# Kernel tuning notes

Measured on AMD Instinct MI355X. Metric: run time of the kernel, lower is better.

Reference implementation:

```python
import jax, jax.numpy as jnp
import numpy as np

TOTAL_WORDS = 10000
EMBED_LEN = 100
SEQ_LEN = 80
UNITS = 512
BATCH = 1024


def gru_layer(x_seq, Wx, Wh, b):
    """Keras GRU (reset_after=True), x_seq: [T, B, D] -> ys: [T, B, U]."""
    bi, br = b[0], b[1]  # input bias, recurrent bias, each [3U]
    U = Wh.shape[0]

    def step(h, x_t):
        gx = x_t @ Wx + bi            # [B, 3U]
        gh = h @ Wh + br              # [B, 3U]
        xz, xr, xh = gx[:, :U], gx[:, U:2 * U], gx[:, 2 * U:]
        hz, hr, hn = gh[:, :U], gh[:, U:2 * U], gh[:, 2 * U:]
        z = jax.nn.sigmoid(xz + hz)
        r = jax.nn.sigmoid(xr + hr)
        hh = jnp.tanh(xh + r * hn)
        h_new = z * h + (1.0 - z) * hh
        return h_new, h_new

    h0 = jnp.zeros((x_seq.shape[1], U), dtype=x_seq.dtype)
    _, ys = jax.lax.scan(step, h0, x_seq)
    return ys


def setup_inputs() -> dict:
    key = jax.random.key(0)
    ks = jax.random.split(key, 10)
    tokens = jax.random.randint(ks[0], (BATCH, SEQ_LEN), 0, TOTAL_WORDS, dtype=jnp.int32)
    s_e = 1.0 / np.sqrt(EMBED_LEN)
    s_u = 1.0 / np.sqrt(UNITS)
    emb = jax.random.normal(ks[1], (TOTAL_WORDS, EMBED_LEN), jnp.float32) * 0.05
    Wx1 = jax.random.normal(ks[2], (EMBED_LEN, 3 * UNITS), jnp.float32) * s_e
    Wh1 = jax.random.normal(ks[3], (UNITS, 3 * UNITS), jnp.float32) * s_u
    b1 = jnp.zeros((2, 3 * UNITS), jnp.float32)
    Wx2 = jax.random.normal(ks[4], (UNITS, 3 * UNITS), jnp.float32) * s_u
    Wh2 = jax.random.normal(ks[5], (UNITS, 3 * UNITS), jnp.float32) * s_u
    b2 = jnp.zeros((2, 3 * UNITS), jnp.float32)
    Wfc = jax.random.normal(ks[6], (UNITS, 1), jnp.float32) * s_u
    bfc = jnp.zeros((1,), jnp.float32)
    return {"tokens": tokens, "emb": emb, "Wx1": Wx1, "Wh1": Wh1, "b1": b1,
            "Wx2": Wx2, "Wh2": Wh2, "b2": b2, "Wfc": Wfc, "bfc": bfc}


def reference(tokens, emb, Wx1, Wh1, b1, Wx2, Wh2, b2, Wfc, bfc):
    x = emb[tokens]                       # [B, T, E]
    x = jnp.transpose(x, (1, 0, 2))       # [T, B, E] (scan over time)
    ys1 = gru_layer(x, Wx1, Wh1, b1)      # [T, B, U] return_sequences
    ys2 = gru_layer(ys1, Wx2, Wh2, b2)    # [T, B, U]
    h_last = ys2[-1]                      # [B, U] (last timestep only)
    logits = h_last @ Wfc + bfc           # [B, 1]
    return jax.nn.sigmoid(logits)
```

## Files before the change

kernel.cpp:

```cpp
#include <hip/hip_runtime.h>
#include <hip/hip_bf16.h>
#include <math.h>

typedef float f32x4 __attribute__((ext_vector_type(4)));
typedef int   ix4  __attribute__((ext_vector_type(4)));

#define MFMAI8(a,b,c) __builtin_amdgcn_mfma_i32_16x16x64_i8(a,b,c,0,0,0)

constexpr int BATCH = 1024, SEQ = 80, EMB = 100, U = 512;
constexpr int KC1 = 10;
constexpr int KC2 = 16;
constexpr float EMBMAX = 0.32f;
constexpr float INV127SQ = 1.f / 16129.f;

__device__ __forceinline__ float sigf_(float x) {
  return __builtin_amdgcn_rcpf(1.f + __expf(-x));
}
__device__ __forceinline__ float tanhf_(float x) {
  return fmaf(2.f, __builtin_amdgcn_rcpf(1.f + __expf(-2.f * x)), -1.f);
}

__global__ void k_colmax(const float* __restrict__ Wh1, const float* __restrict__ Wx1,
                         const float* __restrict__ Wh2, const float* __restrict__ Wx2,
                         float* __restrict__ scales) {
  int idx = blockIdx.x * 256 + threadIdx.x;
  if (idx >= 4 * 8 * 1536) return;
  int col = idx % 1536;
  int rest = idx / 1536;
  int kseg = rest & 7, m = rest >> 3;
  const float* W = (m == 0) ? Wh1 : (m == 1) ? Wx1 : (m == 2) ? Wh2 : Wx2;
  int Klim = (m == 1) ? EMB : 512;
  int k0 = kseg * 64, k1 = min(k0 + 64, Klim);
  float mx = 0.f;
  for (int k = k0; k < k1; ++k) mx = fmaxf(mx, fabsf(W[(size_t)k * 1536 + col]));
  if (k1 > k0) atomicMax((int*)&scales[m * 1536 + col], __float_as_int(mx));
}

__global__ void k_pack_i8(const float* __restrict__ WH, const float* __restrict__ WX,
                          const float* __restrict__ scH, const float* __restrict__ scX,
                          signed char* __restrict__ out, int KCH, int KCX, int KXr) {
  int c = blockIdx.x * 256 + threadIdx.x;
  int KC = KCH + KCX;
  if (c >= 32 * KC * 3 * 64) return;
  int lane = c & 63;
  int rest = c >> 6;
  int g = rest % 3; rest /= 3;
  int kc = rest % KC;
  int lb = rest / KC;
  int col = g * 512 + lb * 16 + (lane & 15);
  int kl = (lane >> 4) * 16;
  float sH = 127.f / fmaxf(scH[col], 1e-12f);
  float sX = 127.f / fmaxf(scX[col], 1e-12f);
  ix4 v;
  signed char* vb = (signed char*)&v;
#pragma unroll
  for (int e = 0; e < 16; ++e) {
    int q = 0;
    if (kc < KCH) {
      int k = kc * 64 + kl + e;
      q = (int)rintf(WH[(size_t)k * 1536 + col] * sH);
    } else {
      int kx = (kc - KCH) * 64 + kl + e;
      if (kx < KXr) q = (int)rintf(WX[(size_t)kx * 1536 + col] * sX);
    }
    vb[e] = (signed char)q;
  }
  *(ix4*)(out + (size_t)c * 16) = v;
}

__global__ void k_emb_quant(const float* __restrict__ in, signed char* __restrict__ out) {
  int idx = blockIdx.x * 256 + threadIdx.x;
  if (idx >= 10000 * 128) return;
  int r = idx >> 7, c = idx & 127;
  int q = 0;
  if (c < EMB) {
    float x = in[r * EMB + c] * (127.f / EMBMAX);
    q = (int)rintf(fminf(127.f, fmaxf(-127.f, x)));
  }
  out[idx] = (signed char)q;
}

__device__ __forceinline__ unsigned llc_read(unsigned* p) {
  unsigned v;
  asm volatile("global_load_dword %0, %1, off sc0 sc1\n\ts_waitcnt vmcnt(0)"
               : "=v"(v) : "v"(p) : "memory");
  return v;
}

__device__ __forceinline__ void bar_slow(unsigned* cnt, unsigned tgt) {
  __syncthreads();
  if (threadIdx.x == 0) {
    __builtin_amdgcn_fence(__ATOMIC_RELEASE, "agent");
    __hip_atomic_fetch_add(cnt, 1u, __ATOMIC_RELAXED, __HIP_MEMORY_SCOPE_AGENT);
    while (__hip_atomic_fetch_add(cnt, 0u, __ATOMIC_RELAXED, __HIP_MEMORY_SCOPE_AGENT) < tgt)
      __builtin_amdgcn_s_sleep(1);
    __builtin_amdgcn_fence(__ATOMIC_ACQUIRE, "agent");
  }
  __syncthreads();
}

__device__ __forceinline__ void bar_fast(unsigned* cnt, unsigned tgt) {
  asm volatile("s_waitcnt vmcnt(0)" ::: "memory");
  __syncthreads();
  if (threadIdx.x == 0) {
    __hip_atomic_fetch_add(cnt, 1u, __ATOMIC_RELAXED, __HIP_MEMORY_SCOPE_AGENT);
    while (llc_read(cnt) < tgt) __builtin_amdgcn_s_sleep(1);
    asm volatile("buffer_inv sc0\n\ts_waitcnt vmcnt(0)" ::: "memory");
  }
  __syncthreads();
}

__global__ __launch_bounds__(512, 2)
void k_gru_persist(const int* __restrict__ tokens, const signed char* __restrict__ embq,
                   const signed char* __restrict__ wf1, const signed char* __restrict__ wf2,
                   const float* __restrict__ b1, const float* __restrict__ b2,
                   const float* __restrict__ scales,
                   signed char* __restrict__ h1b0, signed char* __restrict__ h1b1,
                   signed char* __restrict__ h2b0, signed char* __restrict__ h2b1,
                   const float* __restrict__ Wfc, const float* __restrict__ bfc,
                   float* __restrict__ out, unsigned* __restrict__ bar) {
  __shared__ __attribute__((aligned(16))) signed char wt1[KC1 * 3 * 1024];
  __shared__ __attribute__((aligned(16))) signed char wt2[KC2 * 3 * 1024];
  __shared__ int fastsh;

  const int bid = blockIdx.x, tid = threadIdx.x;
  const int g = bid & 7, lb = bid >> 3;
  const int u0 = lb * 16, r0 = g * 128;
  unsigned* cnt = bar + g * 64;
  unsigned* xslot = bar + 512;

  {
    const ix4* s1 = (const ix4*)(wf1 + (size_t)lb * KC1 * 3 * 1024);
    ix4* d1 = (ix4*)wt1;
    for (int i = tid; i < KC1 * 3 * 64; i += 512) d1[i] = s1[i];
    const ix4* s2 = (const ix4*)(wf2 + (size_t)lb * KC2 * 3 * 1024);
    ix4* d2 = (ix4*)wt2;
    for (int i = tid; i < KC2 * 3 * 64; i += 512) d2[i] = s2[i];
  }

  {
    unsigned xcc = 0;
    asm volatile("s_getreg_b32 %0, hwreg(HW_REG_XCC_ID)" : "=s"(xcc));
    if (tid == 0)
      __hip_atomic_store(&xslot[bid], xcc + 1u, __ATOMIC_RELAXED, __HIP_MEMORY_SCOPE_AGENT);
    bar_slow(cnt, 32u);
    if (tid == 0) {
      unsigned x0 = __hip_atomic_load(&xslot[g], __ATOMIC_RELAXED, __HIP_MEMORY_SCOPE_AGENT);
      int f = (x0 != 0u);
      for (int i = 1; i < 32; ++i)
        f &= (__hip_atomic_load(&xslot[i * 8 + g], __ATOMIC_RELAXED, __HIP_MEMORY_SCOPE_AGENT) == x0);
      fastsh = f;
    }
    __syncthreads();
  }
  const bool fastbar = (fastsh != 0);

  const int wv = tid >> 6, lane = tid & 63, ln = lane & 15, quad = lane >> 4;
  const int rw0 = r0 + wv * 16;
  const int lofs = lane * 16;
  const int kq = quad * 16;

  const int u = u0 + ln;
  const float* sc_h1 = scales, *sc_x1 = scales + 1536, *sc_h2 = scales + 3072, *sc_x2 = scales + 4608;
  const float fz1h = sc_h1[u] * INV127SQ,        fz1x = sc_x1[u] * (EMBMAX * INV127SQ);
  const float fr1h = sc_h1[512 + u] * INV127SQ,  fr1x = sc_x1[512 + u] * (EMBMAX * INV127SQ);
  const float fn1h = sc_h1[1024 + u] * INV127SQ, fn1x = sc_x1[1024 + u] * (EMBMAX * INV127SQ);
  const float fz2h = sc_h2[u] * INV127SQ,        fz2x = sc_x2[u] * INV127SQ;
  const float fr2h = sc_h2[512 + u] * INV127SQ,  fr2x = sc_x2[512 + u] * INV127SQ;
  const float fn2h = sc_h2[1024 + u] * INV127SQ, fn2x = sc_x2[1024 + u] * INV127SQ;
  const float bz1 = b1[u] + b1[1536 + u],       br1 = b1[512 + u] + b1[2048 + u];
  const float bn1x = b1[1024 + u],              bn1h = b1[2560 + u];
  const float bz2 = b2[u] + b2[1536 + u],       br2 = b2[512 + u] + b2[2048 + u];
  const float bn2x = b2[1024 + u],              bn2h = b2[2560 + u];
  const size_t wb8 = (size_t)(u >> 6) * 65536 + (u & 63);

  float h1st[4] = {0.f, 0.f, 0.f, 0.f};
  float h2st[4] = {0.f, 0.f, 0.f, 0.f};
  unsigned tgt = 64u;

#pragma unroll 1
  for (int s = 0; s <= SEQ; ++s) {
    const signed char* h1r = (s & 1) ? h1b0 : h1b1;
    signed char*       h1w = (s & 1) ? h1b1 : h1b0;
    const signed char* h2r = (s & 1) ? h2b1 : h2b0;
    signed char*       h2w = (s & 1) ? h2b0 : h2b1;

    ix4 z1h, z1x, r1h, r1x, n1h, n1x, z2h, z2x, r2h, r2x, n2h, n2x;
    z1h = z1x = r1h = r1x = n1h = n1x = (ix4){0, 0, 0, 0};
    z2h = z2x = r2h = r2x = n2h = n2x = (ix4){0, 0, 0, 0};

#pragma unroll
    for (int kc = 0; kc < 8; ++kc) {
      ix4 a = *(const ix4*)(h1r + (size_t)kc * 65536 + (rw0 + ln) * 64 + kq);
      z1h = MFMAI8(a, *(const ix4*)(wt1 + (kc * 3 + 0) * 1024 + lofs), z1h);
      r1h = MFMAI8(a, *(const ix4*)(wt1 + (kc * 3 + 1) * 1024 + lofs), r1h);
      n1h = MFMAI8(a, *(const ix4*)(wt1 + (kc * 3 + 2) * 1024 + lofs), n1h);
      z2x = MFMAI8(a, *(const ix4*)(wt2 + ((8 + kc) * 3 + 0) * 1024 + lofs), z2x);
      r2x = MFMAI8(a, *(const ix4*)(wt2 + ((8 + kc) * 3 + 1) * 1024 + lofs), r2x);
      n2x = MFMAI8(a, *(const ix4*)(wt2 + ((8 + kc) * 3 + 2) * 1024 + lofs), n2x);
    }
#pragma unroll
    for (int kc = 0; kc < 8; ++kc) {
      ix4 a = *(const ix4*)(h2r + (size_t)kc * 65536 + (rw0 + ln) * 64 + kq);
      z2h = MFMAI8(a, *(const ix4*)(wt2 + (kc * 3 + 0) * 1024 + lofs), z2h);
      r2h = MFMAI8(a, *(const ix4*)(wt2 + (kc * 3 + 1) * 1024 + lofs), r2h);
      n2h = MFMAI8(a, *(const ix4*)(wt2 + (kc * 3 + 2) * 1024 + lofs), n2h);
    }
    {
      int se = (s < SEQ) ? s : SEQ - 1;
      int tok = tokens[(size_t)(rw0 + ln) * SEQ + se];
#pragma unroll
      for (int kc = 0; kc < 2; ++kc) {
        ix4 a = *(const ix4*)(embq + (size_t)tok * 128 + kc * 64 + kq);
        z1x = MFMAI8(a, *(const ix4*)(wt1 + ((8 + kc) * 3 + 0) * 1024 + lofs), z1x);
        r1x = MFMAI8(a, *(const ix4*)(wt1 + ((8 + kc) * 3 + 1) * 1024 + lofs), r1x);
        n1x = MFMAI8(a, *(const ix4*)(wt1 + ((8 + kc) * 3 + 2) * 1024 + lofs), n1x);
      }
    }

    if (s < SEQ) {
#pragma unroll
      for (int i = 0; i < 4; ++i) {
        int row = rw0 + quad * 4 + i;
        float z = sigf_(fmaf(fz1h, (float)z1h[i], fmaf(fz1x, (float)z1x[i], bz1)));
        float r = sigf_(fmaf(fr1h, (float)r1h[i], fmaf(fr1x, (float)r1x[i], br1)));
        float hh = tanhf_(fmaf(fn1x, (float)n1x[i], bn1x) +
                          r * fmaf(fn1h, (float)n1h[i], bn1h));
        float hn = hh + z * (h1st[i] - hh);
        h1st[i] = hn;
        h1w[wb8 + (size_t)row * 64] = (signed char)(int)rintf(hn * 127.f);
      }
    }
    if (s >= 1) {
#pragma unroll
      for (int i = 0; i < 4; ++i) {
        int row = rw0 + quad * 4 + i;
        float z = sigf_(fmaf(fz2h, (float)z2h[i], fmaf(fz2x, (float)z2x[i], bz2)));
        float r = sigf_(fmaf(fr2h, (float)r2h[i], fmaf(fr2x, (float)r2x[i], br2)));
        float hh = tanhf_(fmaf(fn2x, (float)n2x[i], bn2x) +
                          r * fmaf(fn2h, (float)n2h[i], bn2h));
        float hn = hh + z * (h2st[i] - hh);
        h2st[i] = hn;
        h2w[wb8 + (size_t)row * 64] = (signed char)(int)rintf(hn * 127.f);
      }
    }

    if (fastbar) bar_fast(cnt, tgt);
    else         bar_slow(cnt, tgt);
    tgt += 32u;
  }

  if (lb < 8) {
    int row = r0 + lb * 16 + wv * 2 + (lane >> 5);
    int l32 = lane & 31;
    float sfc = 0.f;
#pragma unroll
    for (int k = l32; k < U; k += 32)
      sfc += (float)h2b1[(size_t)(k >> 6) * 65536 + row * 64 + (k & 63)] * Wfc[k];
#pragma unroll
    for (int off = 16; off; off >>= 1) sfc += __shfl_down(sfc, off, 32);
    if (l32 == 0) out[row] = sigf_(sfc * (1.f / 127.f) + bfc[0]);
  }
}

extern "C" void kernel_launch(void* const* d_in, const int* in_sizes, int n_in,
                              void* d_out, int out_size, void* d_ws, size_t ws_size,
                              hipStream_t stream) {
  const int*   tokens = (const int*)d_in[0];
  const float* emb = (const float*)d_in[1];
  const float* Wx1 = (const float*)d_in[2];
  const float* Wh1 = (const float*)d_in[3];
  const float* b1  = (const float*)d_in[4];
  const float* Wx2 = (const float*)d_in[5];
  const float* Wh2 = (const float*)d_in[6];
  const float* b2  = (const float*)d_in[7];
  const float* Wfc = (const float*)d_in[8];
  const float* bfc = (const float*)d_in[9];
  float* out = (float*)d_out;

  signed char* wf1  = (signed char*)d_ws;
  signed char* wf2  = wf1 + 983040;
  signed char* embq = wf2 + 1572864;
  float* scales     = (float*)(embq + 1280000);
  signed char* h1b0 = (signed char*)scales + 24576;
  signed char* h1b1 = h1b0 + 524288;
  signed char* h2b0 = h1b1 + 524288;
  signed char* h2b1 = h2b0 + 524288;
  unsigned* bar = (unsigned*)(h2b1 + 524288);

  hipMemsetAsync(scales, 0, 24576 + (size_t)4 * 524288 + 3072, stream);

  k_colmax<<<(4 * 8 * 1536 + 255) / 256, 256, 0, stream>>>(Wh1, Wx1, Wh2, Wx2, scales);
  k_pack_i8<<<(32 * KC1 * 3 * 64 + 255) / 256, 256, 0, stream>>>(
      Wh1, Wx1, scales, scales + 1536, wf1, 8, 2, EMB);
  k_pack_i8<<<(32 * KC2 * 3 * 64 + 255) / 256, 256, 0, stream>>>(
      Wh2, Wx2, scales + 3072, scales + 4608, wf2, 8, 8, U);
  k_emb_quant<<<(10000 * 128 + 255) / 256, 256, 0, stream>>>(emb, embq);

  void* args[] = {(void*)&tokens, (void*)&embq, (void*)&wf1, (void*)&wf2,
                  (void*)&b1, (void*)&b2, (void*)&scales,
                  (void*)&h1b0, (void*)&h1b1, (void*)&h2b0, (void*)&h2b1,
                  (void*)&Wfc, (void*)&bfc, (void*)&out, (void*)&bar};
  hipLaunchCooperativeKernel((void*)k_gru_persist, dim3(256), dim3(512), args, 0, stream);
}
```

Baseline: 579.0 us.

## Repartition persistent GRU into 16 row-groups, keep layer-1 weights in registers, fuse prep kernels

The persistent kernel now uses 16 batch-row groups of 64 rows, each with 16 blocks, in place of 8 groups of 128 rows with 32 blocks. Each wave covers one of two 16-unit slices, so a block caches two layer-2 weight slices in LDS. Layer-1 weights (30 fragments) move into VGPRs instead of LDS, and each barrier group shrinks to 16 blocks. The three prep kernels (two packs and the embedding quantize) merge into one launch, the embedding quantize writes 4 bytes per thread, and the kernel zeroes the h1 initial buffer itself so the large memset shrinks. The aim is fewer participants per grid barrier, less LDS traffic for layer 1 and fewer launches, at the cost of register pressure that could reduce occupancy under launch_bounds(512,2).

```diff
diff --git a/kernel.cpp b/kernel.cpp
--- a/kernel.cpp
+++ b/kernel.cpp
@@ -36,18 +36,19 @@
   if (k1 > k0) atomicMax((int*)&scales[m * 1536 + col], __float_as_int(mx));
 }
 
-__global__ void k_pack_i8(const float* __restrict__ WH, const float* __restrict__ WX,
-                          const float* __restrict__ scH, const float* __restrict__ scX,
-                          signed char* __restrict__ out, int KCH, int KCX, int KXr) {
-  int c = blockIdx.x * 256 + threadIdx.x;
+__device__ __forceinline__ void pack_one(const float* __restrict__ WH,
+                                         const float* __restrict__ WX,
+                                         const float* __restrict__ scH,
+                                         const float* __restrict__ scX,
+                                         signed char* __restrict__ out,
+                                         int KCH, int KCX, int KXr, int c) {
   int KC = KCH + KCX;
-  if (c >= 32 * KC * 3 * 64) return;
   int lane = c & 63;
   int rest = c >> 6;
   int g = rest % 3; rest /= 3;
   int kc = rest % KC;
-  int lb = rest / KC;
-  int col = g * 512 + lb * 16 + (lane & 15);
+  int u16 = rest / KC;
+  int col = g * 512 + u16 * 16 + (lane & 15);
   int kl = (lane >> 4) * 16;
   float sH = 127.f / fmaxf(scH[col], 1e-12f);
   float sX = 127.f / fmaxf(scX[col], 1e-12f);
@@ -68,16 +69,35 @@
   *(ix4*)(out + (size_t)c * 16) = v;
 }
 
-__global__ void k_emb_quant(const float* __restrict__ in, signed char* __restrict__ out) {
-  int idx = blockIdx.x * 256 + threadIdx.x;
-  if (idx >= 10000 * 128) return;
-  int r = idx >> 7, c = idx & 127;
-  int q = 0;
-  if (c < EMB) {
-    float x = in[r * EMB + c] * (127.f / EMBMAX);
-    q = (int)rintf(fminf(127.f, fmaxf(-127.f, x)));
-  }
-  out[idx] = (signed char)q;
+__global__ void k_prep(const float* __restrict__ Wh1, const float* __restrict__ Wx1,
+                       const float* __restrict__ Wh2, const float* __restrict__ Wx2,
+                       const float* __restrict__ scales,
+                       signed char* __restrict__ wf1, signed char* __restrict__ wf2,
+                       const float* __restrict__ emb, signed char* __restrict__ embq) {
+  int b = blockIdx.x, tid = threadIdx.x;
+  if (b < 240) {
+    int c = b * 256 + tid;
+    if (c < 61440) pack_one(Wh1, Wx1, scales, scales + 1536, wf1, 8, 2, EMB, c);
+  } else if (b < 624) {
+    int c = (b - 240) * 256 + tid;
+    if (c < 98304) pack_one(Wh2, Wx2, scales + 3072, scales + 4608, wf2, 8, 8, U, c);
+  } else {
+    int idx = (b - 624) * 256 + tid;
+    if (idx < 320000) {
+      int r = idx >> 5, c4 = (idx & 31) * 4;
+      char q[4];
+#pragma unroll
+      for (int j = 0; j < 4; ++j) {
+        int c = c4 + j, v = 0;
+        if (c < EMB) {
+          float x = emb[r * EMB + c] * (127.f / EMBMAX);
+          v = (int)rintf(fminf(127.f, fmaxf(-127.f, x)));
+        }
+        q[j] = (char)v;
+      }
+      *(int*)(embq + (size_t)r * 128 + c4) = *(int*)q;
+    }
+  }
 }
 
 __device__ __forceinline__ unsigned llc_read(unsigned* p) {
@@ -119,48 +139,58 @@
                    signed char* __restrict__ h2b0, signed char* __restrict__ h2b1,
                    const float* __restrict__ Wfc, const float* __restrict__ bfc,
                    float* __restrict__ out, unsigned* __restrict__ bar) {
-  __shared__ __attribute__((aligned(16))) signed char wt1[KC1 * 3 * 1024];
-  __shared__ __attribute__((aligned(16))) signed char wt2[KC2 * 3 * 1024];
+  __shared__ __attribute__((aligned(16))) signed char wt2[2 * KC2 * 3 * 1024];
   __shared__ int fastsh;
 
   const int bid = blockIdx.x, tid = threadIdx.x;
-  const int g = bid & 7, lb = bid >> 3;
-  const int u0 = lb * 16, r0 = g * 128;
+  const int g = bid & 15, lb = bid >> 4;
+  const int r0 = g * 64;
   unsigned* cnt = bar + g * 64;
-  unsigned* xslot = bar + 512;
+  unsigned* xslot = bar + 1024;
 
   {
-    const ix4* s1 = (const ix4*)(wf1 + (size_t)lb * KC1 * 3 * 1024);
-    ix4* d1 = (ix4*)wt1;
-    for (int i = tid; i < KC1 * 3 * 64; i += 512) d1[i] = s1[i];
-    const ix4* s2 = (const ix4*)(wf2 + (size_t)lb * KC2 * 3 * 1024);
+    ix4* hz = (ix4*)(h1b0 + (size_t)bid * 8192);
+    hz[tid] = (ix4){0, 0, 0, 0};
+  }
+
+  {
+    const ix4* s2 = (const ix4*)(wf2 + (size_t)lb * 6144 * 16);
     ix4* d2 = (ix4*)wt2;
-    for (int i = tid; i < KC2 * 3 * 64; i += 512) d2[i] = s2[i];
-  }
+    for (int i = tid; i < 6144; i += 512) d2[i] = s2[i];
+  }
+
+  const int wv = tid >> 6, lane = tid & 63, ln = lane & 15, quad = lane >> 4;
+  const int rt = wv >> 1, uh = wv & 1;
+  const int u16 = lb * 2 + uh;
+  const int rw0 = r0 + rt * 16;
+  const int kq = quad * 16;
+
+  ix4 w1[30];
+  {
+    const ix4* s1 = (const ix4*)(wf1 + (size_t)u16 * KC1 * 3 * 1024);
+#pragma unroll
+    for (int f = 0; f < 30; ++f) w1[f] = s1[f * 64 + lane];
+  }
+  const signed char* wt2h = wt2 + uh * (KC2 * 3 * 1024) + lane * 16;
 
   {
     unsigned xcc = 0;
     asm volatile("s_getreg_b32 %0, hwreg(HW_REG_XCC_ID)" : "=s"(xcc));
     if (tid == 0)
       __hip_atomic_store(&xslot[bid], xcc + 1u, __ATOMIC_RELAXED, __HIP_MEMORY_SCOPE_AGENT);
-    bar_slow(cnt, 32u);
+    bar_slow(cnt, 16u);
     if (tid == 0) {
       unsigned x0 = __hip_atomic_load(&xslot[g], __ATOMIC_RELAXED, __HIP_MEMORY_SCOPE_AGENT);
       int f = (x0 != 0u);
-      for (int i = 1; i < 32; ++i)
-        f &= (__hip_atomic_load(&xslot[i * 8 + g], __ATOMIC_RELAXED, __HIP_MEMORY_SCOPE_AGENT) == x0);
+      for (int j = 1; j < 16; ++j)
+        f &= (__hip_atomic_load(&xslot[g + 16 * j], __ATOMIC_RELAXED, __HIP_MEMORY_SCOPE_AGENT) == x0);
       fastsh = f;
     }
     __syncthreads();
   }
   const bool fastbar = (fastsh != 0);
 
-  const int wv = tid >> 6, lane = tid & 63, ln = lane & 15, quad = lane >> 4;
-  const int rw0 = r0 + wv * 16;
-  const int lofs = lane * 16;
-  const int kq = quad * 16;
-
-  const int u = u0 + ln;
+  const int u = u16 * 16 + ln;
   const float* sc_h1 = scales, *sc_x1 = scales + 1536, *sc_h2 = scales + 3072, *sc_x2 = scales + 4608;
   const float fz1h = sc_h1[u] * INV127SQ,        fz1x = sc_x1[u] * (EMBMAX * INV127SQ);
   const float fr1h = sc_h1[512 + u] * INV127SQ,  fr1x = sc_x1[512 + u] * (EMBMAX * INV127SQ);
@@ -176,7 +206,7 @@
 
   float h1st[4] = {0.f, 0.f, 0.f, 0.f};
   float h2st[4] = {0.f, 0.f, 0.f, 0.f};
-  unsigned tgt = 64u;
+  unsigned tgt = 32u;
 
 #pragma unroll 1
   for (int s = 0; s <= SEQ; ++s) {
@@ -192,19 +222,19 @@
 #pragma unroll
     for (int kc = 0; kc < 8; ++kc) {
       ix4 a = *(const ix4*)(h1r + (size_t)kc * 65536 + (rw0 + ln) * 64 + kq);
-      z1h = MFMAI8(a, *(const ix4*)(wt1 + (kc * 3 + 0) * 1024 + lofs), z1h);
-      r1h = MFMAI8(a, *(const ix4*)(wt1 + (kc * 3 + 1) * 1024 + lofs), r1h);
-      n1h = MFMAI8(a, *(const ix4*)(wt1 + (kc * 3 + 2) * 1024 + lofs), n1h);
-      z2x = MFMAI8(a, *(const ix4*)(wt2 + ((8 + kc) * 3 + 0) * 1024 + lofs), z2x);
-      r2x = MFMAI8(a, *(const ix4*)(wt2 + ((8 + kc) * 3 + 1) * 1024 + lofs), r2x);
-      n2x = MFMAI8(a, *(const ix4*)(wt2 + ((8 + kc) * 3 + 2) * 1024 + lofs), n2x);
+      z1h = MFMAI8(a, w1[kc * 3 + 0], z1h);
+      r1h = MFMAI8(a, w1[kc * 3 + 1], r1h);
+      n1h = MFMAI8(a, w1[kc * 3 + 2], n1h);
+      z2x = MFMAI8(a, *(const ix4*)(wt2h + ((8 + kc) * 3 + 0) * 1024), z2x);
+      r2x = MFMAI8(a, *(const ix4*)(wt2h + ((8 + kc) * 3 + 1) * 1024), r2x);
+      n2x = MFMAI8(a, *(const ix4*)(wt2h + ((8 + kc) * 3 + 2) * 1024), n2x);
     }
 #pragma unroll
     for (int kc = 0; kc < 8; ++kc) {
       ix4 a = *(const ix4*)(h2r + (size_t)kc * 65536 + (rw0 + ln) * 64 + kq);
-      z2h = MFMAI8(a, *(const ix4*)(wt2 + (kc * 3 + 0) * 1024 + lofs), z2h);
-      r2h = MFMAI8(a, *(const ix4*)(wt2 + (kc * 3 + 1) * 1024 + lofs), r2h);
-      n2h = MFMAI8(a, *(const ix4*)(wt2 + (kc * 3 + 2) * 1024 + lofs), n2h);
+      z2h = MFMAI8(a, *(const ix4*)(wt2h + (kc * 3 + 0) * 1024), z2h);
+      r2h = MFMAI8(a, *(const ix4*)(wt2h + (kc * 3 + 1) * 1024), r2h);
+      n2h = MFMAI8(a, *(const ix4*)(wt2h + (kc * 3 + 2) * 1024), n2h);
     }
     {
       int se = (s < SEQ) ? s : SEQ - 1;
@@ -212,9 +242,9 @@
 #pragma unroll
       for (int kc = 0; kc < 2; ++kc) {
         ix4 a = *(const ix4*)(embq + (size_t)tok * 128 + kc * 64 + kq);
-        z1x = MFMAI8(a, *(const ix4*)(wt1 + ((8 + kc) * 3 + 0) * 1024 + lofs), z1x);
-        r1x = MFMAI8(a, *(const ix4*)(wt1 + ((8 + kc) * 3 + 1) * 1024 + lofs), r1x);
-        n1x = MFMAI8(a, *(const ix4*)(wt1 + ((8 + kc) * 3 + 2) * 1024 + lofs), n1x);
+        z1x = MFMAI8(a, w1[(8 + kc) * 3 + 0], z1x);
+        r1x = MFMAI8(a, w1[(8 + kc) * 3 + 1], r1x);
+        n1x = MFMAI8(a, w1[(8 + kc) * 3 + 2], n1x);
       }
     }
 
@@ -247,19 +277,20 @@
 
     if (fastbar) bar_fast(cnt, tgt);
     else         bar_slow(cnt, tgt);
-    tgt += 32u;
-  }
-
-  if (lb < 8) {
-    int row = r0 + lb * 16 + wv * 2 + (lane >> 5);
-    int l32 = lane & 31;
+    tgt += 16u;
+  }
+
+  if (wv < 4) {
+    int row = r0 + lb * 4 + wv;
     float sfc = 0.f;
 #pragma unroll
-    for (int k = l32; k < U; k += 32)
-      sfc += (float)h2b1[(size_t)(k >> 6) * 65536 + row * 64 + (k & 63)] * Wfc[k];
-#pragma unroll
-    for (int off = 16; off; off >>= 1) sfc += __shfl_down(sfc, off, 32);
-    if (l32 == 0) out[row] = sigf_(sfc * (1.f / 127.f) + bfc[0]);
+    for (int j = 0; j < 8; ++j) {
+      int k = j * 64 + lane;
+      sfc += (float)h2b1[(size_t)j * 65536 + row * 64 + lane] * Wfc[k];
+    }
+#pragma unroll
+    for (int off = 32; off; off >>= 1) sfc += __shfl_down(sfc, off, 64);
+    if (lane == 0) out[row] = sigf_(sfc * (1.f / 127.f) + bfc[0]);
   }
 }
 
@@ -282,20 +313,16 @@
   signed char* wf2  = wf1 + 983040;
   signed char* embq = wf2 + 1572864;
   float* scales     = (float*)(embq + 1280000);
-  signed char* h1b0 = (signed char*)scales + 24576;
+  unsigned* bar     = (unsigned*)((signed char*)scales + 24576);
+  signed char* h1b0 = (signed char*)bar + 8192;
   signed char* h1b1 = h1b0 + 524288;
   signed char* h2b0 = h1b1 + 524288;
   signed char* h2b1 = h2b0 + 524288;
-  unsigned* bar = (unsigned*)(h2b1 + 524288);
-
-  hipMemsetAsync(scales, 0, 24576 + (size_t)4 * 524288 + 3072, stream);
+
+  hipMemsetAsync(scales, 0, 24576 + 8192, stream);
 
   k_colmax<<<(4 * 8 * 1536 + 255) / 256, 256, 0, stream>>>(Wh1, Wx1, Wh2, Wx2, scales);
-  k_pack_i8<<<(32 * KC1 * 3 * 64 + 255) / 256, 256, 0, stream>>>(
-      Wh1, Wx1, scales, scales + 1536, wf1, 8, 2, EMB);
-  k_pack_i8<<<(32 * KC2 * 3 * 64 + 255) / 256, 256, 0, stream>>>(
-      Wh2, Wx2, scales + 3072, scales + 4608, wf2, 8, 8, U);
-  k_emb_quant<<<(10000 * 128 + 255) / 256, 256, 0, stream>>>(emb, embq);
+  k_prep<<<1874, 256, 0, stream>>>(Wh1, Wx1, Wh2, Wx2, scales, wf1, wf2, emb, embq);
 
   void* args[] = {(void*)&tokens, (void*)&embq, (void*)&wf1, (void*)&wf2,
                   (void*)&b1, (void*)&b2, (void*)&scales,
```

Result: faster. 555.5 us (-4.1%).
